# Kernel tuning notes

Measured on AMD Instinct MI355X. Metric: run time of the kernel, lower is better.

## Reference

```python
import jax, jax.numpy as jnp
import numpy as np

EMBED_DIM = 256
NUM_HEADS = 8
HEAD_DIM = EMBED_DIM // NUM_HEADS
ADJ_CHANNELS = 4
B, N = 8, 1024


def setup_inputs() -> dict:
    key = jax.random.key(0)
    ks = jax.random.split(key, 12)
    s = 1.0 / np.sqrt(EMBED_DIM)
    sa = 1.0 / np.sqrt(ADJ_CHANNELS)
    return {
        "x": jax.random.normal(ks[0], (B, N, EMBED_DIM), dtype=jnp.float32),
        "adj": jax.random.uniform(ks[1], (B, N, N, ADJ_CHANNELS), dtype=jnp.float32),
        "Wq": jax.random.uniform(ks[2], (EMBED_DIM, EMBED_DIM), jnp.float32, -s, s),
        "bq": jnp.zeros((EMBED_DIM,), jnp.float32),
        "Wk": jax.random.uniform(ks[3], (EMBED_DIM, EMBED_DIM), jnp.float32, -s, s),
        "bk": jnp.zeros((EMBED_DIM,), jnp.float32),
        "Wv": jax.random.uniform(ks[4], (EMBED_DIM, EMBED_DIM), jnp.float32, -s, s),
        "bv": jnp.zeros((EMBED_DIM,), jnp.float32),
        "Wo": jax.random.uniform(ks[5], (EMBED_DIM, EMBED_DIM), jnp.float32, -s, s),
        "bo": jnp.zeros((EMBED_DIM,), jnp.float32),
        "Wa": jax.random.uniform(ks[6], (ADJ_CHANNELS, NUM_HEADS), jnp.float32, -sa, sa),
        "ba": jnp.zeros((NUM_HEADS,), jnp.float32),
    }


def reference(x, adj, Wq, bq, Wk, bk, Wv, bv, Wo, bo, Wa, ba):
    Bs, Ns, E = x.shape
    H, D = NUM_HEADS, HEAD_DIM
    def heads(W, b):
        return (x @ W + b).reshape(Bs, Ns, H, D).transpose(0, 2, 1, 3)  # [B,H,N,D]
    Q, K, V = heads(Wq, bq), heads(Wk, bk), heads(Wv, bv)
    # adjacency-derived additive bias: [B,N,N,C] -> [B,N,N,H] -> [B,H,N,N]
    bias = jnp.moveaxis(adj @ Wa + ba, -1, 1)
    scores = jnp.einsum("bhnd,bhmd->bhnm", Q, K) / np.sqrt(D) + bias
    attn = jax.nn.softmax(scores, axis=-1)
    ctx = jnp.einsum("bhnm,bhmd->bhnd", attn, V)  # [B,H,N,D]
    ctx = ctx.transpose(0, 2, 1, 3).reshape(Bs, Ns, E)
    return ctx @ Wo + bo + x
```

## Files before the change

### kernel.cpp

```cpp
#include <hip/hip_runtime.h>
#include <hip/hip_bf16.h>

#define BATCH 8
#define SEQ   1024
#define EMB   256
#define NH    8
#define HD    32
#define QSCALE 0.2550030053f

typedef __attribute__((ext_vector_type(8))) short short8;
typedef __attribute__((ext_vector_type(4))) float floatx4;

__device__ __forceinline__ ushort f2bf(float f) {
    __hip_bfloat16 h = __float2bfloat16(f);
    return *reinterpret_cast<ushort*>(&h);
}

__device__ __forceinline__ float bf2f(ushort u) {
    unsigned v = ((unsigned)u) << 16;
    return __builtin_bit_cast(float, v);
}

__device__ __forceinline__ void gload_lds16(const float4* g, float4* l) {
    __builtin_amdgcn_global_load_lds(
        (const __attribute__((address_space(1))) unsigned int*)g,
        (__attribute__((address_space(3))) unsigned int*)l, 16, 0, 0);
}

__global__ __launch_bounds__(256) void prep_kernel(
    const float* __restrict__ Wq, const float* __restrict__ Wk,
    const float* __restrict__ Wv, const float* __restrict__ Wo,
    ushort* __restrict__ Wqt, ushort* __restrict__ Wkt,
    ushort* __restrict__ Wvt, ushort* __restrict__ Wot)
{
    __shared__ float tilebuf[32][33];
    const int blk = blockIdx.x;
    const int mat = blk >> 6, tile = blk & 63;
    const int ti = tile >> 3, tj = tile & 7;
    const float* W = (mat == 0) ? Wq : (mat == 1) ? Wk : (mat == 2) ? Wv : Wo;
    ushort* Wt = (mat == 0) ? Wqt : (mat == 1) ? Wkt : (mat == 2) ? Wvt : Wot;
    const float scale = (mat == 0) ? QSCALE : 1.0f;

    const int tx = threadIdx.x & 31, ty = threadIdx.x >> 5;
    #pragma unroll
    for (int p = 0; p < 4; ++p)
        tilebuf[ty + p * 8][tx] = W[(size_t)(ti * 32 + ty + p * 8) * EMB + tj * 32 + tx];
    __syncthreads();
    #pragma unroll
    for (int p = 0; p < 4; ++p)
        Wt[(size_t)(tj * 32 + ty + p * 8) * EMB + ti * 32 + tx] =
            f2bf(tilebuf[tx][ty + p * 8] * scale);
}

__global__ __launch_bounds__(256) void qkv_gemm(
    const float* __restrict__ x,
    const ushort* __restrict__ Wqt, const ushort* __restrict__ Wkt,
    const ushort* __restrict__ Wvt,
    const float* __restrict__ bq, const float* __restrict__ bk,
    const float* __restrict__ bv,
    ushort* __restrict__ Qb, ushort* __restrict__ Kb, ushort* __restrict__ Vt)
{
    const int mat = blockIdx.y;
    const ushort* __restrict__ Wt = (mat == 0) ? Wqt : (mat == 1) ? Wkt : Wvt;
    const float* __restrict__ bias = (mat == 0) ? bq : (mat == 1) ? bk : bv;
    const float bscale = (mat == 0) ? QSCALE : 1.0f;

    const int w = threadIdx.x >> 6, lane = threadIdx.x & 63;
    const int quad = lane >> 4, l16 = lane & 15;
    const int row0 = blockIdx.x * 64 + w * 16;

    floatx4 acc[16];
    #pragma unroll
    for (int i = 0; i < 16; ++i) acc[i] = (floatx4){0.f, 0.f, 0.f, 0.f};

    const float* __restrict__ xrow = x + (size_t)(row0 + l16) * EMB + quad * 8;

    #pragma unroll
    for (int ks = 0; ks < 8; ++ks) {
        const float4 xa0 = *(const float4*)(xrow + ks * 32);
        const float4 xa1 = *(const float4*)(xrow + ks * 32 + 4);
        ushort au[8] = {f2bf(xa0.x), f2bf(xa0.y), f2bf(xa0.z), f2bf(xa0.w),
                        f2bf(xa1.x), f2bf(xa1.y), f2bf(xa1.z), f2bf(xa1.w)};
        const short8 a = *(const short8*)au;
        #pragma unroll
        for (int i = 0; i < 16; ++i) {
            const short8 bf = *(const short8*)(Wt + (size_t)(i * 16 + l16) * EMB + ks * 32 + quad * 8);
            acc[i] = __builtin_amdgcn_mfma_f32_16x16x32_bf16(a, bf, acc[i], 0, 0, 0);
        }
    }

    const int gr0 = row0 + quad * 4;
    if (mat < 2) {
        ushort* __restrict__ dst = (mat == 0) ? Qb : Kb;
        #pragma unroll
        for (int i = 0; i < 16; ++i) {
            const int c = i * 16 + l16, h = c >> 5, d = c & (HD - 1);
            const float bb = bias[c] * bscale;
            #pragma unroll
            for (int r = 0; r < 4; ++r) {
                const int gr = gr0 + r, b = gr >> 10, n = gr & (SEQ - 1);
                dst[(size_t)(b * NH + h) * SEQ * HD + (size_t)(n >> 4) * 512
                    + (d >> 3) * 128 + (n & 15) * 8 + (d & 7)] = f2bf(acc[i][r] + bb);
            }
        }
    } else {
        const int b = gr0 >> 10, n0 = gr0 & (SEQ - 1);
        const int keyblk = n0 >> 5, j0 = n0 & 31;
        const int sg = (j0 & 15) >> 2, si0 = (j0 & 16) ? 4 : 0;
        #pragma unroll
        for (int i = 0; i < 16; ++i) {
            const int c = i * 16 + l16, h = c >> 5, d = c & (HD - 1);
            const float bb = bias[c];
            ushort4 t4;
            t4.x = f2bf(acc[i][0] + bb); t4.y = f2bf(acc[i][1] + bb);
            t4.z = f2bf(acc[i][2] + bb); t4.w = f2bf(acc[i][3] + bb);
            *(ushort4*)(Vt + (size_t)(b * NH + h) * SEQ * HD + (size_t)keyblk * 1024
                        + (d >> 4) * 512 + sg * 128 + (d & 15) * 8 + si0) = t4;
        }
    }
}

__global__ __launch_bounds__(512) void attn_kernel(
    const ushort* __restrict__ Qb, const ushort* __restrict__ Kb,
    const ushort* __restrict__ Vt, const float* __restrict__ adj,
    const float* __restrict__ Wa, const float* __restrict__ ba,
    ushort* __restrict__ cp, float* __restrict__ lsum)
{
    __shared__ float4 Atile[2][16][65];
    const int tid = threadIdx.x, h = tid >> 6, lane = tid & 63;
    const int quad = lane >> 4, l16 = lane & 15;
    const int q0 = blockIdx.x * 16, b = blockIdx.y, z = blockIdx.z;
    const int bh = b * NH + h;
    const int kz = z * 512;

    const float LOG2E = 1.4426950408889634f;
    const float wa0 = Wa[0 * NH + h] * LOG2E, wa1 = Wa[1 * NH + h] * LOG2E;
    const float wa2 = Wa[2 * NH + h] * LOG2E, wa3 = Wa[3 * NH + h] * LOG2E;
    const float bah = ba[h] * LOG2E;

    const short8 aq = *(const short8*)(Qb + (size_t)bh * SEQ * HD
                                      + (size_t)blockIdx.x * 512 + lane * 8);

    floatx4 o0 = {0.f, 0.f, 0.f, 0.f}, o1 = {0.f, 0.f, 0.f, 0.f};
    float lacc = 0.f;

    const float4* __restrict__ adjb = (const float4*)adj + (size_t)b * SEQ * SEQ;
    const float4* __restrict__ asrc0 = adjb + (size_t)(q0 + 2 * h)     * SEQ + kz + lane;
    const float4* __restrict__ asrc1 = adjb + (size_t)(q0 + 2 * h + 1) * SEQ + kz + lane;

    const ushort* __restrict__ Kbase = Kb + (size_t)bh * SEQ * HD + lane * 8;
    const ushort* __restrict__ Vbase = Vt + (size_t)bh * SEQ * HD + lane * 8;

    gload_lds16(asrc0, &Atile[0][2 * h][0]);
    gload_lds16(asrc1, &Atile[0][2 * h + 1][0]);
    __syncthreads();

    for (int it = 0; it < 8; ++it) {
        const int cur = it & 1;
        const int key0 = kz + it * 64;

        if (it < 7) {
            gload_lds16(asrc0 + (it + 1) * 64, &Atile[cur ^ 1][2 * h][0]);
            gload_lds16(asrc1 + (it + 1) * 64, &Atile[cur ^ 1][2 * h + 1][0]);
        }

        const ushort* kp = Kbase + (size_t)(key0 >> 4) * 512;
        const short8 k0 = *(const short8*)(kp);
        const short8 k1 = *(const short8*)(kp + 512);
        const short8 k2 = *(const short8*)(kp + 1024);
        const short8 k3 = *(const short8*)(kp + 1536);
        const floatx4 zz = {0.f, 0.f, 0.f, 0.f};
        floatx4 s0 = __builtin_amdgcn_mfma_f32_16x16x32_bf16(k0, aq, zz, 0, 0, 0);
        floatx4 s1 = __builtin_amdgcn_mfma_f32_16x16x32_bf16(k1, aq, zz, 0, 0, 0);
        floatx4 s2 = __builtin_amdgcn_mfma_f32_16x16x32_bf16(k2, aq, zz, 0, 0, 0);
        floatx4 s3 = __builtin_amdgcn_mfma_f32_16x16x32_bf16(k3, aq, zz, 0, 0, 0);

        ushort pu0[8], pu1[8];
        #pragma unroll
        for (int r = 0; r < 4; ++r) {
            const int col = 4 * quad + r;
            const float4 a0 = Atile[cur][l16][col];
            const float4 a1 = Atile[cur][l16][16 + col];
            const float4 a2 = Atile[cur][l16][32 + col];
            const float4 a3 = Atile[cur][l16][48 + col];
            const float b0 = fmaf(a0.x, wa0, fmaf(a0.y, wa1, fmaf(a0.z, wa2, fmaf(a0.w, wa3, bah))));
            const float b1 = fmaf(a1.x, wa0, fmaf(a1.y, wa1, fmaf(a1.z, wa2, fmaf(a1.w, wa3, bah))));
            const float b2 = fmaf(a2.x, wa0, fmaf(a2.y, wa1, fmaf(a2.z, wa2, fmaf(a2.w, wa3, bah))));
            const float b3 = fmaf(a3.x, wa0, fmaf(a3.y, wa1, fmaf(a3.z, wa2, fmaf(a3.w, wa3, bah))));
            const float p0 = __builtin_amdgcn_exp2f(s0[r] + b0);
            const float p1 = __builtin_amdgcn_exp2f(s1[r] + b1);
            const float p2 = __builtin_amdgcn_exp2f(s2[r] + b2);
            const float p3 = __builtin_amdgcn_exp2f(s3[r] + b3);
            lacc += (p0 + p1) + (p2 + p3);
            pu0[r]     = f2bf(p0);
            pu0[4 + r] = f2bf(p1);
            pu1[r]     = f2bf(p2);
            pu1[4 + r] = f2bf(p3);
        }
        const short8 pf0 = *(const short8*)pu0;
        const short8 pf1 = *(const short8*)pu1;

        const ushort* vp = Vbase + (size_t)(key0 >> 5) * 1024;
        const short8 v00 = *(const short8*)(vp);
        const short8 v10 = *(const short8*)(vp + 512);
        const short8 v01 = *(const short8*)(vp + 1024);
        const short8 v11 = *(const short8*)(vp + 1536);
        o0 = __builtin_amdgcn_mfma_f32_16x16x32_bf16(v00, pf0, o0, 0, 0, 0);
        o1 = __builtin_amdgcn_mfma_f32_16x16x32_bf16(v10, pf0, o1, 0, 0, 0);
        o0 = __builtin_amdgcn_mfma_f32_16x16x32_bf16(v01, pf1, o0, 0, 0, 0);
        o1 = __builtin_amdgcn_mfma_f32_16x16x32_bf16(v11, pf1, o1, 0, 0, 0);

        __syncthreads();
    }

    lacc += __shfl_xor(lacc, 16, 64);
    lacc += __shfl_xor(lacc, 32, 64);

    ushort* __restrict__ cpz = cp + (size_t)z * BATCH * SEQ * EMB;
    float* __restrict__ lsz = lsum + (size_t)z * BATCH * SEQ * NH;
    const size_t grow = (size_t)b * SEQ + q0 + l16;
    ushort4 t0, t1;
    t0.x = f2bf(o0[0]); t0.y = f2bf(o0[1]); t0.z = f2bf(o0[2]); t0.w = f2bf(o0[3]);
    t1.x = f2bf(o1[0]); t1.y = f2bf(o1[1]); t1.z = f2bf(o1[2]); t1.w = f2bf(o1[3]);
    *(ushort4*)(cpz + grow * EMB + h * HD + 4 * quad)      = t0;
    *(ushort4*)(cpz + grow * EMB + h * HD + 16 + 4 * quad) = t1;
    if (quad == 0) lsz[grow * NH + h] = lacc;
}

__global__ __launch_bounds__(256) void outproj_gemm(
    const ushort* __restrict__ cp, const float* __restrict__ lsum,
    const ushort* __restrict__ Wot, const float* __restrict__ bo,
    const float* __restrict__ x, float* __restrict__ out)
{
    const int w = threadIdx.x >> 6, lane = threadIdx.x & 63;
    const int quad = lane >> 4, l16 = lane & 15;
    const int row0 = blockIdx.x * 64 + w * 16;
    const int c0 = blockIdx.y * 128;
    const int arow = row0 + l16;
    const ushort* __restrict__ cp1 = cp + (size_t)BATCH * SEQ * EMB;
    const float* __restrict__ l1  = lsum + (size_t)BATCH * SEQ * NH;

    floatx4 acc[8];
    #pragma unroll
    for (int i = 0; i < 8; ++i) acc[i] = (floatx4){0.f, 0.f, 0.f, 0.f};

    #pragma unroll
    for (int ks = 0; ks < 8; ++ks) {
        const float invl = 1.0f / (lsum[(size_t)arow * NH + ks] + l1[(size_t)arow * NH + ks]);
        const size_t cb = (size_t)arow * EMB + ks * 32 + quad * 8;
        const ushort4 c00 = *(const ushort4*)(cp + cb);
        const ushort4 c01 = *(const ushort4*)(cp + cb + 4);
        const ushort4 c10 = *(const ushort4*)(cp1 + cb);
        const ushort4 c11 = *(const ushort4*)(cp1 + cb + 4);
        ushort au[8] = {
            f2bf((bf2f(c00.x) + bf2f(c10.x)) * invl),
            f2bf((bf2f(c00.y) + bf2f(c10.y)) * invl),
            f2bf((bf2f(c00.z) + bf2f(c10.z)) * invl),
            f2bf((bf2f(c00.w) + bf2f(c10.w)) * invl),
            f2bf((bf2f(c01.x) + bf2f(c11.x)) * invl),
            f2bf((bf2f(c01.y) + bf2f(c11.y)) * invl),
            f2bf((bf2f(c01.z) + bf2f(c11.z)) * invl),
            f2bf((bf2f(c01.w) + bf2f(c11.w)) * invl)};
        const short8 a = *(const short8*)au;
        #pragma unroll
        for (int i = 0; i < 8; ++i) {
            const short8 bfr = *(const short8*)(Wot + (size_t)(c0 + i * 16 + l16) * EMB + ks * 32 + quad * 8);
            acc[i] = __builtin_amdgcn_mfma_f32_16x16x32_bf16(a, bfr, acc[i], 0, 0, 0);
        }
    }

    const int gr0 = row0 + quad * 4;
    #pragma unroll
    for (int i = 0; i < 8; ++i) {
        const int c = c0 + i * 16 + l16;
        const float bov = bo[c];
        #pragma unroll
        for (int r = 0; r < 4; ++r) {
            const size_t idx = (size_t)(gr0 + r) * EMB + c;
            out[idx] = acc[i][r] + bov + x[idx];
        }
    }
}

extern "C" void kernel_launch(void* const* d_in, const int* in_sizes, int n_in,
                              void* d_out, int out_size, void* d_ws, size_t ws_size,
                              hipStream_t stream) {
    const float* x   = (const float*)d_in[0];
    const float* adj = (const float*)d_in[1];
    const float* Wq  = (const float*)d_in[2];
    const float* bq  = (const float*)d_in[3];
    const float* Wk  = (const float*)d_in[4];
    const float* bk  = (const float*)d_in[5];
    const float* Wv  = (const float*)d_in[6];
    const float* bv  = (const float*)d_in[7];
    const float* Wo  = (const float*)d_in[8];
    const float* bo  = (const float*)d_in[9];
    const float* Wa  = (const float*)d_in[10];
    const float* ba  = (const float*)d_in[11];

    const size_t per = (size_t)BATCH * NH * SEQ * HD;
    ushort* Qb  = (ushort*)d_ws;
    ushort* Kb  = Qb + per;
    ushort* Vt  = Kb + per;
    ushort* Wqt = Vt + per;
    ushort* Wkt = Wqt + EMB * EMB;
    ushort* Wvt = Wkt + EMB * EMB;
    ushort* Wot = Wvt + EMB * EMB;
    ushort* cpw = Wot + EMB * EMB;
    float*  ls  = (float*)(cpw + 2 * (size_t)BATCH * SEQ * EMB);

    prep_kernel<<<256, 256, 0, stream>>>(Wq, Wk, Wv, Wo, Wqt, Wkt, Wvt, Wot);
    qkv_gemm<<<dim3(BATCH * SEQ / 64, 3), 256, 0, stream>>>(
        x, Wqt, Wkt, Wvt, bq, bk, bv, Qb, Kb, Vt);
    attn_kernel<<<dim3(SEQ / 16, BATCH, 2), 512, 0, stream>>>(
        Qb, Kb, Vt, adj, Wa, ba, cpw, ls);
    outproj_gemm<<<dim3(BATCH * SEQ / 64, 2), 256, 0, stream>>>(
        cpw, ls, Wot, bo, x, (float*)d_out);
}
```

Before: 285.9 us.

## Pre-swizzle weights, x and attention output into MFMA fragment-major tiles

The prep kernel now writes the transposed bf16 weights in a fragment-major tiled layout. It also gains 512 extra blocks that convert x to bf16 in the same layout. The QKV and output-projection GEMMs can then load each operand fragment as a contiguous lane*8 vector instead of strided row loads, and the QKV kernel no longer converts fp32 x to bf16 three times. The attention kernel writes its partial context in the matching tiled layout for the output projection. The cost is one extra pass over x and an extra workspace buffer, and most of the runtime is likely in the attention kernel, which this barely touches.

```diff
diff --git a/kernel.cpp b/kernel.cpp
--- a/kernel.cpp
+++ b/kernel.cpp
@@ -27,33 +27,51 @@
         (__attribute__((address_space(3))) unsigned int*)l, 16, 0, 0);
 }
 
+
 __global__ __launch_bounds__(256) void prep_kernel(
     const float* __restrict__ Wq, const float* __restrict__ Wk,
     const float* __restrict__ Wv, const float* __restrict__ Wo,
+    const float* __restrict__ x,
     ushort* __restrict__ Wqt, ushort* __restrict__ Wkt,
-    ushort* __restrict__ Wvt, ushort* __restrict__ Wot)
+    ushort* __restrict__ Wvt, ushort* __restrict__ Wot,
+    ushort* __restrict__ xb)
 {
-    __shared__ float tilebuf[32][33];
     const int blk = blockIdx.x;
-    const int mat = blk >> 6, tile = blk & 63;
-    const int ti = tile >> 3, tj = tile & 7;
-    const float* W = (mat == 0) ? Wq : (mat == 1) ? Wk : (mat == 2) ? Wv : Wo;
-    ushort* Wt = (mat == 0) ? Wqt : (mat == 1) ? Wkt : (mat == 2) ? Wvt : Wot;
-    const float scale = (mat == 0) ? QSCALE : 1.0f;
-
-    const int tx = threadIdx.x & 31, ty = threadIdx.x >> 5;
-    #pragma unroll
-    for (int p = 0; p < 4; ++p)
-        tilebuf[ty + p * 8][tx] = W[(size_t)(ti * 32 + ty + p * 8) * EMB + tj * 32 + tx];
-    __syncthreads();
-    #pragma unroll
-    for (int p = 0; p < 4; ++p)
-        Wt[(size_t)(tj * 32 + ty + p * 8) * EMB + ti * 32 + tx] =
-            f2bf(tilebuf[tx][ty + p * 8] * scale);
+    if (blk < 256) {
+        __shared__ float tilebuf[32][33];
+        const int mat = blk >> 6, tile = blk & 63;
+        const int ti = tile >> 3, tj = tile & 7;
+        const float* W = (mat == 0) ? Wq : (mat == 1) ? Wk : (mat == 2) ? Wv : Wo;
+        ushort* Wt = (mat == 0) ? Wqt : (mat == 1) ? Wkt : (mat == 2) ? Wvt : Wot;
+        const float scale = (mat == 0) ? QSCALE : 1.0f;
+
+        const int tx = threadIdx.x & 31, ty = threadIdx.x >> 5;
+        #pragma unroll
+        for (int p = 0; p < 4; ++p)
+            tilebuf[ty + p * 8][tx] = W[(size_t)(ti * 32 + ty + p * 8) * EMB + tj * 32 + tx];
+        __syncthreads();
+        #pragma unroll
+        for (int p = 0; p < 4; ++p) {
+            const int n = tj * 32 + ty + p * 8;
+            const int k = ti * 32 + tx;
+            Wt[(size_t)(n >> 4) * 4096 + (k >> 5) * 512 + ((k >> 3) & 3) * 128
+               + (n & 15) * 8 + (k & 7)] = f2bf(tilebuf[tx][ty + p * 8] * scale);
+        }
+    } else {
+        const int tile = blk - 256;
+        const float* __restrict__ xs = x + (size_t)tile * 16 * EMB;
+        ushort* __restrict__ xd = xb + (size_t)tile * 4096;
+        #pragma unroll
+        for (int j = 0; j < 16; ++j) {
+            const int o = j * 256 + threadIdx.x;
+            const int ks = o >> 9, quad = (o >> 7) & 3, l16 = (o >> 3) & 15, e = o & 7;
+            xd[o] = f2bf(xs[(size_t)l16 * EMB + ks * 32 + quad * 8 + e]);
+        }
+    }
 }
 
 __global__ __launch_bounds__(256) void qkv_gemm(
-    const float* __restrict__ x,
+    const ushort* __restrict__ xb,
     const ushort* __restrict__ Wqt, const ushort* __restrict__ Wkt,
     const ushort* __restrict__ Wvt,
     const float* __restrict__ bq, const float* __restrict__ bk,
@@ -73,18 +91,15 @@
     #pragma unroll
     for (int i = 0; i < 16; ++i) acc[i] = (floatx4){0.f, 0.f, 0.f, 0.f};
 
-    const float* __restrict__ xrow = x + (size_t)(row0 + l16) * EMB + quad * 8;
+    const ushort* __restrict__ xrow = xb + (size_t)(blockIdx.x * 4 + w) * 4096 + lane * 8;
+    const ushort* __restrict__ wrow = Wt + lane * 8;
 
     #pragma unroll
     for (int ks = 0; ks < 8; ++ks) {
-        const float4 xa0 = *(const float4*)(xrow + ks * 32);
-        const float4 xa1 = *(const float4*)(xrow + ks * 32 + 4);
-        ushort au[8] = {f2bf(xa0.x), f2bf(xa0.y), f2bf(xa0.z), f2bf(xa0.w),
-                        f2bf(xa1.x), f2bf(xa1.y), f2bf(xa1.z), f2bf(xa1.w)};
-        const short8 a = *(const short8*)au;
+        const short8 a = *(const short8*)(xrow + ks * 512);
         #pragma unroll
         for (int i = 0; i < 16; ++i) {
-            const short8 bf = *(const short8*)(Wt + (size_t)(i * 16 + l16) * EMB + ks * 32 + quad * 8);
+            const short8 bf = *(const short8*)(wrow + (size_t)i * 4096 + ks * 512);
             acc[i] = __builtin_amdgcn_mfma_f32_16x16x32_bf16(a, bf, acc[i], 0, 0, 0);
         }
     }
@@ -218,12 +233,14 @@
 
     ushort* __restrict__ cpz = cp + (size_t)z * BATCH * SEQ * EMB;
     float* __restrict__ lsz = lsum + (size_t)z * BATCH * SEQ * NH;
-    const size_t grow = (size_t)b * SEQ + q0 + l16;
+    const size_t tbase = ((size_t)b * 64 + blockIdx.x) * 4096 + (size_t)h * 512
+                       + l16 * 32 + 4 * quad;
     ushort4 t0, t1;
     t0.x = f2bf(o0[0]); t0.y = f2bf(o0[1]); t0.z = f2bf(o0[2]); t0.w = f2bf(o0[3]);
     t1.x = f2bf(o1[0]); t1.y = f2bf(o1[1]); t1.z = f2bf(o1[2]); t1.w = f2bf(o1[3]);
-    *(ushort4*)(cpz + grow * EMB + h * HD + 4 * quad)      = t0;
-    *(ushort4*)(cpz + grow * EMB + h * HD + 16 + 4 * quad) = t1;
+    *(ushort4*)(cpz + tbase)      = t0;
+    *(ushort4*)(cpz + tbase + 16) = t1;
+    const size_t grow = (size_t)b * SEQ + q0 + l16;
     if (quad == 0) lsz[grow * NH + h] = lacc;
 }
 
@@ -240,6 +257,9 @@
     const ushort* __restrict__ cp1 = cp + (size_t)BATCH * SEQ * EMB;
     const float* __restrict__ l1  = lsum + (size_t)BATCH * SEQ * NH;
 
+    const size_t tb = (size_t)(blockIdx.x * 4 + w) * 4096 + l16 * 32 + quad * 8;
+    const ushort* __restrict__ wrow = Wot + (size_t)(c0 >> 4) * 4096 + lane * 8;
+
     floatx4 acc[8];
     #pragma unroll
     for (int i = 0; i < 8; ++i) acc[i] = (floatx4){0.f, 0.f, 0.f, 0.f};
@@ -247,11 +267,10 @@
     #pragma unroll
     for (int ks = 0; ks < 8; ++ks) {
         const float invl = 1.0f / (lsum[(size_t)arow * NH + ks] + l1[(size_t)arow * NH + ks]);
-        const size_t cb = (size_t)arow * EMB + ks * 32 + quad * 8;
-        const ushort4 c00 = *(const ushort4*)(cp + cb);
-        const ushort4 c01 = *(const ushort4*)(cp + cb + 4);
-        const ushort4 c10 = *(const ushort4*)(cp1 + cb);
-        const ushort4 c11 = *(const ushort4*)(cp1 + cb + 4);
+        const ushort4 c00 = *(const ushort4*)(cp  + tb + ks * 512);
+        const ushort4 c01 = *(const ushort4*)(cp  + tb + ks * 512 + 4);
+        const ushort4 c10 = *(const ushort4*)(cp1 + tb + ks * 512);
+        const ushort4 c11 = *(const ushort4*)(cp1 + tb + ks * 512 + 4);
         ushort au[8] = {
             f2bf((bf2f(c00.x) + bf2f(c10.x)) * invl),
             f2bf((bf2f(c00.y) + bf2f(c10.y)) * invl),
@@ -264,7 +283,7 @@
         const short8 a = *(const short8*)au;
         #pragma unroll
         for (int i = 0; i < 8; ++i) {
-            const short8 bfr = *(const short8*)(Wot + (size_t)(c0 + i * 16 + l16) * EMB + ks * 32 + quad * 8);
+            const short8 bfr = *(const short8*)(wrow + (size_t)i * 4096 + ks * 512);
             acc[i] = __builtin_amdgcn_mfma_f32_16x16x32_bf16(a, bfr, acc[i], 0, 0, 0);
         }
     }
@@ -307,11 +326,13 @@
     ushort* Wvt = Wkt + EMB * EMB;
     ushort* Wot = Wvt + EMB * EMB;
     ushort* cpw = Wot + EMB * EMB;
-    float*  ls  = (float*)(cpw + 2 * (size_t)BATCH * SEQ * EMB);
-
-    prep_kernel<<<256, 256, 0, stream>>>(Wq, Wk, Wv, Wo, Wqt, Wkt, Wvt, Wot);
+    ushort* xbp = cpw + 2 * (size_t)BATCH * SEQ * EMB;
+    float*  ls  = (float*)(xbp + (size_t)BATCH * SEQ * EMB);
+
+    prep_kernel<<<768, 256, 0, stream>>>(Wq, Wk, Wv, Wo, x,
+                                         Wqt, Wkt, Wvt, Wot, xbp);
     qkv_gemm<<<dim3(BATCH * SEQ / 64, 3), 256, 0, stream>>>(
-        x, Wqt, Wkt, Wvt, bq, bk, bv, Qb, Kb, Vt);
+        xbp, Wqt, Wkt, Wvt, bq, bk, bv, Qb, Kb, Vt);
     attn_kernel<<<dim3(SEQ / 16, BATCH, 2), 512, 0, stream>>>(
         Qb, Kb, Vt, adj, Wa, ba, cpw, ls);
     outproj_gemm<<<dim3(BATCH * SEQ / 64, 2), 256, 0, stream>>>(
```

After: 276.0 us. 1.04x faster.
